# Kernel optimization log

Hardware: AMD Instinct MI355X
Metric: run time of the kernel (lower is better)

Reference implementation:

```python
import jax, jax.numpy as jnp
import numpy as np

NUM_HEADS = 16


def setup_inputs() -> dict:
    key = jax.random.key(0)
    ks = jax.random.split(key, 9)
    B, Nq, Nk = 2, 2048, 2048
    qd, kd, vd = 1024, 1024, 1024
    s = 0.02
    return {
        "query": jax.random.normal(ks[0], (B, Nq, qd), jnp.float32),
        "key": jax.random.normal(ks[1], (B, Nk, kd), jnp.float32),
        "value": jax.random.normal(ks[2], (B, Nk, vd), jnp.float32),
        "Wq": jax.random.normal(ks[3], (qd, qd), jnp.float32) * s,
        "bq": jnp.zeros((qd,), jnp.float32),
        "Wk": jax.random.normal(ks[4], (kd, qd), jnp.float32) * s,
        "bk": jnp.zeros((qd,), jnp.float32),
        "Wv": jax.random.normal(ks[5], (vd, vd), jnp.float32) * s,
        "bv": jnp.zeros((vd,), jnp.float32),
    }


def _split_heads(x, num_heads):
    B, N, D = x.shape
    return x.reshape(B, N, num_heads, D // num_heads).transpose(0, 2, 1, 3)  # [B,H,N,depth]


def reference(query, key, value, Wq, bq, Wk, bk, Wv, bv):
    H = NUM_HEADS
    q = _split_heads(query @ Wq + bq, H)   # [B,H,Nq,dq]
    k = _split_heads(key @ Wk + bk, H)     # [B,H,Nk,dq]
    v = _split_heads(value @ Wv + bv, H)   # [B,H,Nk,dv]
    q_depth = q.shape[-1]
    scores = jnp.einsum('bhqd,bhkd->bhqk', q, k) / jnp.sqrt(jnp.float32(q_depth))
    scores = scores - jnp.max(scores, axis=-1, keepdims=True)
    attn = jax.nn.softmax(scores, axis=-1)  # [B,H,Nq,Nk]
    context = jnp.einsum('bhqk,bhkd->bhqd', attn, v)
    B, _, Nq, dv = context.shape
    context = context.transpose(0, 2, 1, 3).reshape(B, Nq, H * dv)
    return (context, attn)
```

## Files before the change

### kernel.cpp

```cpp
#include <hip/hip_runtime.h>
#include <hip/hip_bf16.h>
#include <stdint.h>

typedef __attribute__((ext_vector_type(4))) float floatx4;
typedef __attribute__((ext_vector_type(8))) short shortx8;

#define NTOK 2048
#define DMODEL 1024
#define NHEAD 16
#define DHEAD 64
#define BATCH 2

static __device__ __forceinline__ unsigned short f2bf(float f) {
    union { float f; unsigned int u; } v; v.f = f;
    return (unsigned short)((v.u + 0x7FFFu + ((v.u >> 16) & 1u)) >> 16);
}

static __device__ __forceinline__ floatx4 mfma16(shortx8 a, shortx8 b, floatx4 c) {
    return __builtin_amdgcn_mfma_f32_16x16x32_bf16(a, b, c, 0, 0, 0);
}

static __device__ __forceinline__ void gl_lds16(const unsigned short* g, unsigned short* l) {
    __builtin_amdgcn_global_load_lds(
        (const __attribute__((address_space(1))) unsigned int*)g,
        (__attribute__((address_space(3))) unsigned int*)l, 16, 0, 0);
}

#define C1 0.18033688f

__global__ void cast_x_kernel(const float* __restrict__ q, const float* __restrict__ k,
                              const float* __restrict__ v,
                              unsigned short* __restrict__ oq, unsigned short* __restrict__ ok,
                              unsigned short* __restrict__ ov) {
    const float* src = blockIdx.y == 0 ? q : (blockIdx.y == 1 ? k : v);
    unsigned short* dst = blockIdx.y == 0 ? oq : (blockIdx.y == 1 ? ok : ov);
    int i = (blockIdx.x * 256 + threadIdx.x) * 8;
    floatx4 a = *(const floatx4*)(src + i);
    floatx4 b = *(const floatx4*)(src + i + 4);
    union { shortx8 s; unsigned short u[8]; } o;
    o.u[0] = f2bf(a[0]); o.u[1] = f2bf(a[1]); o.u[2] = f2bf(a[2]); o.u[3] = f2bf(a[3]);
    o.u[4] = f2bf(b[0]); o.u[5] = f2bf(b[1]); o.u[6] = f2bf(b[2]); o.u[7] = f2bf(b[3]);
    *(shortx8*)(dst + i) = o.s;
}

__global__ void transpose_w_kernel(const float* __restrict__ wq, const float* __restrict__ wk,
                                   const float* __restrict__ wv,
                                   unsigned short* __restrict__ tq, unsigned short* __restrict__ tk,
                                   unsigned short* __restrict__ tv) {
    __shared__ float tile[32][33];
    const float* W = blockIdx.z == 0 ? wq : (blockIdx.z == 1 ? wk : wv);
    unsigned short* T = blockIdx.z == 0 ? tq : (blockIdx.z == 1 ? tk : tv);
    int tx = threadIdx.x, ty = threadIdx.y;
    int bx = blockIdx.x, by = blockIdx.y;
#pragma unroll
    for (int j = 0; j < 4; j++)
        tile[ty + j * 8][tx] = W[(by * 32 + ty + j * 8) * DMODEL + bx * 32 + tx];
    __syncthreads();
#pragma unroll
    for (int j = 0; j < 4; j++)
        T[(bx * 32 + ty + j * 8) * DMODEL + by * 32 + tx] = f2bf(tile[tx][ty + j * 8]);
}

__launch_bounds__(256)
__global__ void proj_gemm_kernel(const unsigned short* __restrict__ xq, const unsigned short* __restrict__ xk,
                                 const unsigned short* __restrict__ xv,
                                 const unsigned short* __restrict__ tq, const unsigned short* __restrict__ tk,
                                 const unsigned short* __restrict__ tv,
                                 const float* __restrict__ bq, const float* __restrict__ bk,
                                 const float* __restrict__ bv,
                                 unsigned short* __restrict__ qh, unsigned short* __restrict__ kh,
                                 unsigned short* __restrict__ vt) {
    int z = blockIdx.z;
    const unsigned short* X = z == 0 ? xq : (z == 1 ? xk : xv);
    const unsigned short* W = z == 0 ? tq : (z == 1 ? tk : tv);
    const float* bias = z == 0 ? bq : (z == 1 ? bk : bv);

    __shared__ unsigned short As[128 * 32];
    __shared__ unsigned short Bs[128 * 32];

    int t = threadIdx.x;
    int lane = t & 63, w = t >> 6;
    int wr = w >> 1, wc = w & 1;
    int r = lane & 15, g = lane >> 4;
    int m0 = blockIdx.y * 128, n0 = blockIdx.x * 128;

    floatx4 acc[4][4];
#pragma unroll
    for (int i = 0; i < 4; i++)
#pragma unroll
        for (int j = 0; j < 4; j++) acc[i][j] = (floatx4){0.f, 0.f, 0.f, 0.f};

    for (int kt = 0; kt < DMODEL; kt += 32) {
#pragma unroll
        for (int i = 0; i < 2; i++) {
            int idx = t + 256 * i;
            int row = idx >> 2, c8 = (idx & 3) * 8;
            gl_lds16(X + (size_t)(m0 + row) * DMODEL + kt + c8, As + idx * 8);
            gl_lds16(W + (size_t)(n0 + row) * DMODEL + kt + c8, Bs + idx * 8);
        }
        __syncthreads();
        shortx8 a[4], b[4];
#pragma unroll
        for (int f = 0; f < 4; f++) {
            a[f] = *(const shortx8*)(As + (wr * 64 + f * 16 + r) * 32 + g * 8);
            b[f] = *(const shortx8*)(Bs + (wc * 64 + f * 16 + r) * 32 + g * 8);
        }
#pragma unroll
        for (int fm = 0; fm < 4; fm++)
#pragma unroll
            for (int fn = 0; fn < 4; fn++)
                acc[fm][fn] = mfma16(a[fm], b[fn], acc[fm][fn]);
        __syncthreads();
    }

    unsigned short* dstQK = (z == 0) ? qh : kh;
#pragma unroll
    for (int fm = 0; fm < 4; fm++) {
#pragma unroll
        for (int fn = 0; fn < 4; fn++) {
            int n = n0 + wc * 64 + fn * 16 + r;
            float bval = bias[n];
            int h = n >> 6, d = n & 63;
#pragma unroll
            for (int reg = 0; reg < 4; reg++) {
                int m = m0 + wr * 64 + fm * 16 + g * 4 + reg;
                int bb = m >> 11, tok = m & 2047;
                unsigned short o = f2bf(acc[fm][fn][reg] + bval);
                if (z < 2)
                    dstQK[(((size_t)(bb * NHEAD + h) * NTOK + tok) * DHEAD) + d] = o;
                else
                    vt[(((size_t)(bb * NHEAD + h) * DHEAD + d) * NTOK) + tok] = o;
            }
        }
    }
}

__launch_bounds__(256, 4)
__global__ void attn_fused_kernel(const unsigned short* __restrict__ Qh,
                                  const unsigned short* __restrict__ Kh,
                                  const unsigned short* __restrict__ Vt,
                                  float* __restrict__ ctx, float* __restrict__ attn) {
    __shared__ __align__(16) unsigned short Kst[2][4096];
    __shared__ __align__(16) unsigned short Aux[2][4096];

    int t = threadIdx.x, lane = t & 63, w = t >> 6, r = lane & 15, g = lane >> 4;

    int bid = blockIdx.y * 64 + blockIdx.x;
    int xcd = bid & 7;
    int j = bid >> 3;
    int bh = xcd * 4 + (j & 3);
    int rest = j >> 2;
    int qb = rest >> 1;
    int role = rest & 1;

    int q0 = qb * 64 + w * 16;
    int qrow = q0 + r;
    int rs = r & 7;

    const unsigned short* Qp = Qh + ((size_t)bh * NTOK + q0) * DHEAD;
    const unsigned short* Kbase = Kh + (size_t)bh * NTOK * DHEAD;
    const unsigned short* Vbase = Vt + (size_t)bh * DHEAD * NTOK;

    shortx8 qf0 = *(const shortx8*)(Qp + r * DHEAD + g * 8);
    shortx8 qf1 = *(const shortx8*)(Qp + r * DHEAD + 32 + g * 8);

    const floatx4 zero = (floatx4){0.f, 0.f, 0.f, 0.f};

    auto STK = [&](int b, int it) {
#pragma unroll
        for (int p = 0; p < 2; ++p) {
            int row = p * 32 + (t >> 3);
            int cb = (t & 7) ^ ((t >> 3) & 7);
            gl_lds16(Kbase + ((size_t)(it * 64 + row)) * DHEAD + cb * 8,
                     Kst[b] + p * 2048 + t * 8);
        }
    };
    auto STV = [&](int b, int it) {
#pragma unroll
        for (int p = 0; p < 2; ++p) {
            int row = p * 32 + (t >> 3);
            int cb = (t & 7) ^ ((t >> 3) & 7);
            gl_lds16(Vbase + (size_t)row * NTOK + it * 64 + cb * 8,
                     Aux[b] + p * 2048 + t * 8);
        }
    };
    auto KF = [&](int b, int tq, int h) -> shortx8 {
        return *(const shortx8*)(Kst[b] + (tq * 16 + r) * 64 + 8 * (((h * 4) + g) ^ rs));
    };
    auto VF = [&](int b, int dt, int h4) -> shortx8 {
        return *(const shortx8*)(Aux[b] + (dt * 16 + r) * 64 + 8 * ((h4 + g) ^ rs));
    };

    if (role == 0) {
        floatx4 pv0 = zero, pv1 = zero, pv2 = zero, pv3 = zero;
        float sm = 0.f;
        const bool hi = (g >= 2);
        const int srcA = (r + ((g & 1) << 5)) << 2;
        const int srcB = srcA + 64;

        STK(0, 0); STV(0, 0);
        __syncthreads();
        for (int it = 0; it < 32; ++it) {
            int cur = it & 1, nxt = cur ^ 1;
            if (it < 31) { STK(nxt, it + 1); STV(nxt, it + 1); }
#pragma unroll
            for (int half = 0; half < 2; ++half) {
                unsigned int p01t0, p23t0, p01t1, p23t1;
                {
                    floatx4 sc = mfma16(KF(cur, half * 2, 0), qf0, zero);
                    sc = mfma16(KF(cur, half * 2, 1), qf1, sc);
                    float e0 = exp2f(C1 * sc[0]), e1 = exp2f(C1 * sc[1]);
                    float e2 = exp2f(C1 * sc[2]), e3 = exp2f(C1 * sc[3]);
                    sm += (e0 + e1) + (e2 + e3);
                    asm("v_cvt_pk_bf16_f32 %0, %1, %2" : "=v"(p01t0) : "v"(e0), "v"(e1));
                    asm("v_cvt_pk_bf16_f32 %0, %1, %2" : "=v"(p23t0) : "v"(e2), "v"(e3));
                }
                {
                    floatx4 sc = mfma16(KF(cur, half * 2 + 1, 0), qf0, zero);
                    sc = mfma16(KF(cur, half * 2 + 1, 1), qf1, sc);
                    float e0 = exp2f(C1 * sc[0]), e1 = exp2f(C1 * sc[1]);
                    float e2 = exp2f(C1 * sc[2]), e3 = exp2f(C1 * sc[3]);
                    sm += (e0 + e1) + (e2 + e3);
                    asm("v_cvt_pk_bf16_f32 %0, %1, %2" : "=v"(p01t1) : "v"(e0), "v"(e1));
                    asm("v_cvt_pk_bf16_f32 %0, %1, %2" : "=v"(p23t1) : "v"(e2), "v"(e3));
                }
                int b0a = __builtin_amdgcn_ds_bpermute(srcA, (int)p01t0);
                int b0b = __builtin_amdgcn_ds_bpermute(srcA, (int)p01t1);
                int b1a = __builtin_amdgcn_ds_bpermute(srcA, (int)p23t0);
                int b1b = __builtin_amdgcn_ds_bpermute(srcA, (int)p23t1);
                int b2a = __builtin_amdgcn_ds_bpermute(srcB, (int)p01t0);
                int b2b = __builtin_amdgcn_ds_bpermute(srcB, (int)p01t1);
                int b3a = __builtin_amdgcn_ds_bpermute(srcB, (int)p23t0);
                int b3b = __builtin_amdgcn_ds_bpermute(srcB, (int)p23t1);
                union { unsigned int u[4]; shortx8 s8; } pbu;
                pbu.u[0] = (unsigned)(hi ? b0b : b0a);
                pbu.u[1] = (unsigned)(hi ? b1b : b1a);
                pbu.u[2] = (unsigned)(hi ? b2b : b2a);
                pbu.u[3] = (unsigned)(hi ? b3b : b3a);
                pv0 = mfma16(VF(cur, 0, half * 4), pbu.s8, pv0);
                pv1 = mfma16(VF(cur, 1, half * 4), pbu.s8, pv1);
                pv2 = mfma16(VF(cur, 2, half * 4), pbu.s8, pv2);
                pv3 = mfma16(VF(cur, 3, half * 4), pbu.s8, pv3);
            }
            __syncthreads();
        }
        float tot = sm;
        tot += __shfl_xor(tot, 16, 64);
        tot += __shfl_xor(tot, 32, 64);
        float inv = 1.0f / tot;
        float* ctx_row =
            ctx + ((size_t)((bh >> 4) * NTOK + qrow)) * DMODEL + (bh & 15) * DHEAD + g * 4;
        *(floatx4*)(ctx_row) = pv0 * inv;
        *(floatx4*)(ctx_row + 16) = pv1 * inv;
        *(floatx4*)(ctx_row + 32) = pv2 * inv;
        *(floatx4*)(ctx_row + 48) = pv3 * inv;
    } else {
        float sm = 0.f;
        STK(0, 0);
        __syncthreads();
        for (int it = 0; it < 32; ++it) {
            int cur = it & 1, nxt = cur ^ 1;
            if (it < 31) STK(nxt, it + 1);
#pragma unroll
            for (int tq = 0; tq < 4; ++tq) {
                floatx4 sc = mfma16(KF(cur, tq, 0), qf0, zero);
                sc = mfma16(KF(cur, tq, 1), qf1, sc);
                sm += (exp2f(C1 * sc[0]) + exp2f(C1 * sc[1])) +
                      (exp2f(C1 * sc[2]) + exp2f(C1 * sc[3]));
            }
            __syncthreads();
        }
        float tot = sm;
        tot += __shfl_xor(tot, 16, 64);
        tot += __shfl_xor(tot, 32, 64);
        float nl2s = -__log2f(tot);

        float(*pw)[64] = (float(*)[64])((char*)Aux + (size_t)w * 4096);
        float* attn_base = attn + ((size_t)bh * NTOK + q0) * NTOK;

        STK(0, 0);
        asm volatile("s_waitcnt vmcnt(0)" ::: "memory");
        __builtin_amdgcn_sched_barrier(0);
        __builtin_amdgcn_s_barrier();
        __builtin_amdgcn_sched_barrier(0);

        for (int it = 0; it < 32; ++it) {
            int cur = it & 1, nxt = cur ^ 1;
            if (it < 31) STK(nxt, it + 1);
            int kk0 = it * 64;
#pragma unroll
            for (int tq = 0; tq < 4; ++tq) {
                floatx4 sc = mfma16(KF(cur, tq, 0), qf0, zero);
                sc = mfma16(KF(cur, tq, 1), qf1, sc);
                float e0 = exp2f(fmaf(C1, sc[0], nl2s));
                float e1 = exp2f(fmaf(C1, sc[1], nl2s));
                float e2 = exp2f(fmaf(C1, sc[2], nl2s));
                float e3 = exp2f(fmaf(C1, sc[3], nl2s));
                int x_ = (tq * 4 + g) ^ r;
                *(floatx4*)&pw[r][4 * x_] = (floatx4){e0, e1, e2, e3};
            }
#pragma unroll
            for (int sID = 0; sID < 4; ++sID) {
                int row = 4 * sID + g;
                floatx4 vvv = *(const floatx4*)&pw[row][4 * (r ^ row)];
                __builtin_nontemporal_store(
                    vvv, (floatx4*)(attn_base + (size_t)row * NTOK + kk0 + 4 * r));
            }
            if (it < 31) {
                asm volatile("s_waitcnt vmcnt(4)" ::: "memory");
                __builtin_amdgcn_sched_barrier(0);
                __builtin_amdgcn_s_barrier();
                __builtin_amdgcn_sched_barrier(0);
            }
        }
    }
}

extern "C" void kernel_launch(void* const* d_in, const int* in_sizes, int n_in,
                              void* d_out, int out_size, void* d_ws, size_t ws_size,
                              hipStream_t stream) {
    const float* query = (const float*)d_in[0];
    const float* key   = (const float*)d_in[1];
    const float* value = (const float*)d_in[2];
    const float* Wq = (const float*)d_in[3];
    const float* bq = (const float*)d_in[4];
    const float* Wk = (const float*)d_in[5];
    const float* bk = (const float*)d_in[6];
    const float* Wv = (const float*)d_in[7];
    const float* bv = (const float*)d_in[8];

    const size_t NX = (size_t)BATCH * NTOK * DMODEL;
    const size_t NW = (size_t)DMODEL * DMODEL;

    unsigned short* ws = (unsigned short*)d_ws;
    unsigned short* Xq = ws;
    unsigned short* Xk = Xq + NX;
    unsigned short* Xv = Xk + NX;
    unsigned short* Tq = Xv + NX;
    unsigned short* Tk = Tq + NW;
    unsigned short* Tv = Tk + NW;
    unsigned short* Qh = Tv + NW;
    unsigned short* Kh = Qh + NX;
    unsigned short* Vt = Kh + NX;

    float* ctx = (float*)d_out;
    float* attn = ctx + NX;

    cast_x_kernel<<<dim3(2048, 3), 256, 0, stream>>>(query, key, value, Xq, Xk, Xv);
    transpose_w_kernel<<<dim3(32, 32, 3), dim3(32, 8), 0, stream>>>(Wq, Wk, Wv, Tq, Tk, Tv);
    proj_gemm_kernel<<<dim3(8, 32, 3), 256, 0, stream>>>(Xq, Xk, Xv, Tq, Tk, Tv,
                                                         bq, bk, bv, Qh, Kh, Vt);
    attn_fused_kernel<<<dim3(64, 32), 256, 0, stream>>>(Qh, Kh, Vt, ctx, attn);
}
```

Baseline: 249.6 us.

## Merge attn-writer blocks to handle two query tiles per block

The attention-probability writer blocks now each cover two 64-row query tiles. The row-sum pass computes both tiles' scores from a single K stream, and two write passes follow. The grid shrinks from 2048 to 1536 blocks: 1024 context blocks and 512 writer blocks. This halves the extra K reads and barriers in the sum pass and balances work between the two roles, at the cost of more register pressure and fewer blocks to spread across CUs.

```diff
diff --git a/kernel.cpp b/kernel.cpp
--- a/kernel.cpp
+++ b/kernel.cpp
@@ -145,24 +145,16 @@
 
     int t = threadIdx.x, lane = t & 63, w = t >> 6, r = lane & 15, g = lane >> 4;
 
-    int bid = blockIdx.y * 64 + blockIdx.x;
+    int bid = blockIdx.x;
     int xcd = bid & 7;
     int j = bid >> 3;
     int bh = xcd * 4 + (j & 3);
-    int rest = j >> 2;
-    int qb = rest >> 1;
-    int role = rest & 1;
-
-    int q0 = qb * 64 + w * 16;
-    int qrow = q0 + r;
+    int unit = j >> 2;
+
     int rs = r & 7;
 
-    const unsigned short* Qp = Qh + ((size_t)bh * NTOK + q0) * DHEAD;
     const unsigned short* Kbase = Kh + (size_t)bh * NTOK * DHEAD;
     const unsigned short* Vbase = Vt + (size_t)bh * DHEAD * NTOK;
-
-    shortx8 qf0 = *(const shortx8*)(Qp + r * DHEAD + g * 8);
-    shortx8 qf1 = *(const shortx8*)(Qp + r * DHEAD + 32 + g * 8);
 
     const floatx4 zero = (floatx4){0.f, 0.f, 0.f, 0.f};
 
@@ -191,7 +183,13 @@
         return *(const shortx8*)(Aux[b] + (dt * 16 + r) * 64 + 8 * ((h4 + g) ^ rs));
     };
 
-    if (role == 0) {
+    if (unit < 32) {
+        int q0 = unit * 64 + w * 16;
+        int qrow = q0 + r;
+        const unsigned short* Qp = Qh + ((size_t)bh * NTOK + q0) * DHEAD;
+        shortx8 qf0 = *(const shortx8*)(Qp + r * DHEAD + g * 8);
+        shortx8 qf1 = *(const shortx8*)(Qp + r * DHEAD + 32 + g * 8);
+
         floatx4 pv0 = zero, pv1 = zero, pv2 = zero, pv3 = zero;
         float sm = 0.f;
         const bool hi = (g >= 2);
@@ -255,7 +253,18 @@
         *(floatx4*)(ctx_row + 32) = pv2 * inv;
         *(floatx4*)(ctx_row + 48) = pv3 * inv;
     } else {
-        float sm = 0.f;
+        int pr = unit - 32;
+        int q0a = (pr * 2) * 64 + w * 16;
+        int q0b = q0a + 64;
+
+        const unsigned short* Qpa = Qh + ((size_t)bh * NTOK + q0a) * DHEAD;
+        const unsigned short* Qpb = Qh + ((size_t)bh * NTOK + q0b) * DHEAD;
+        shortx8 qf0a = *(const shortx8*)(Qpa + r * DHEAD + g * 8);
+        shortx8 qf1a = *(const shortx8*)(Qpa + r * DHEAD + 32 + g * 8);
+        shortx8 qf0b = *(const shortx8*)(Qpb + r * DHEAD + g * 8);
+        shortx8 qf1b = *(const shortx8*)(Qpb + r * DHEAD + 32 + g * 8);
+
+        float sma = 0.f, smb = 0.f;
         STK(0, 0);
         __syncthreads();
         for (int it = 0; it < 32; ++it) {
@@ -263,55 +272,72 @@
             if (it < 31) STK(nxt, it + 1);
 #pragma unroll
             for (int tq = 0; tq < 4; ++tq) {
-                floatx4 sc = mfma16(KF(cur, tq, 0), qf0, zero);
-                sc = mfma16(KF(cur, tq, 1), qf1, sc);
-                sm += (exp2f(C1 * sc[0]) + exp2f(C1 * sc[1])) +
-                      (exp2f(C1 * sc[2]) + exp2f(C1 * sc[3]));
+                floatx4 sa = mfma16(KF(cur, tq, 0), qf0a, zero);
+                sa = mfma16(KF(cur, tq, 1), qf1a, sa);
+                floatx4 sb = mfma16(KF(cur, tq, 0), qf0b, zero);
+                sb = mfma16(KF(cur, tq, 1), qf1b, sb);
+                sma += (exp2f(C1 * sa[0]) + exp2f(C1 * sa[1])) +
+                       (exp2f(C1 * sa[2]) + exp2f(C1 * sa[3]));
+                smb += (exp2f(C1 * sb[0]) + exp2f(C1 * sb[1])) +
+                       (exp2f(C1 * sb[2]) + exp2f(C1 * sb[3]));
             }
             __syncthreads();
         }
-        float tot = sm;
-        tot += __shfl_xor(tot, 16, 64);
-        tot += __shfl_xor(tot, 32, 64);
-        float nl2s = -__log2f(tot);
+        float tota = sma, totb = smb;
+        tota += __shfl_xor(tota, 16, 64);
+        tota += __shfl_xor(tota, 32, 64);
+        totb += __shfl_xor(totb, 16, 64);
+        totb += __shfl_xor(totb, 32, 64);
+        float nl2sa = -__log2f(tota);
+        float nl2sb = -__log2f(totb);
 
         float(*pw)[64] = (float(*)[64])((char*)Aux + (size_t)w * 4096);
-        float* attn_base = attn + ((size_t)bh * NTOK + q0) * NTOK;
-
-        STK(0, 0);
-        asm volatile("s_waitcnt vmcnt(0)" ::: "memory");
-        __builtin_amdgcn_sched_barrier(0);
-        __builtin_amdgcn_s_barrier();
-        __builtin_amdgcn_sched_barrier(0);
-
-        for (int it = 0; it < 32; ++it) {
-            int cur = it & 1, nxt = cur ^ 1;
-            if (it < 31) STK(nxt, it + 1);
-            int kk0 = it * 64;
-#pragma unroll
-            for (int tq = 0; tq < 4; ++tq) {
-                floatx4 sc = mfma16(KF(cur, tq, 0), qf0, zero);
-                sc = mfma16(KF(cur, tq, 1), qf1, sc);
-                float e0 = exp2f(fmaf(C1, sc[0], nl2s));
-                float e1 = exp2f(fmaf(C1, sc[1], nl2s));
-                float e2 = exp2f(fmaf(C1, sc[2], nl2s));
-                float e3 = exp2f(fmaf(C1, sc[3], nl2s));
-                int x_ = (tq * 4 + g) ^ r;
-                *(floatx4*)&pw[r][4 * x_] = (floatx4){e0, e1, e2, e3};
+
+#pragma unroll 1
+        for (int half = 0; half < 2; ++half) {
+            int q0 = half == 0 ? q0a : q0b;
+            float nl2s = half == 0 ? nl2sa : nl2sb;
+            float* attn_base = attn + ((size_t)bh * NTOK + q0) * NTOK;
+
+            STK(0, 0);
+            asm volatile("s_waitcnt vmcnt(0)" ::: "memory");
+            __builtin_amdgcn_sched_barrier(0);
+            __builtin_amdgcn_s_barrier();
+            __builtin_amdgcn_sched_barrier(0);
+
+            for (int it = 0; it < 32; ++it) {
+                int cur = it & 1, nxt = cur ^ 1;
+                if (it < 31) STK(nxt, it + 1);
+                int kk0 = it * 64;
+#pragma unroll
+                for (int tq = 0; tq < 4; ++tq) {
+                    floatx4 sc = mfma16(KF(cur, tq, 0), half == 0 ? qf0a : qf0b, zero);
+                    sc = mfma16(KF(cur, tq, 1), half == 0 ? qf1a : qf1b, sc);
+                    float e0 = exp2f(fmaf(C1, sc[0], nl2s));
+                    float e1 = exp2f(fmaf(C1, sc[1], nl2s));
+                    float e2 = exp2f(fmaf(C1, sc[2], nl2s));
+                    float e3 = exp2f(fmaf(C1, sc[3], nl2s));
+                    int x_ = (tq * 4 + g) ^ r;
+                    *(floatx4*)&pw[r][4 * x_] = (floatx4){e0, e1, e2, e3};
+                }
+#pragma unroll
+                for (int sID = 0; sID < 4; ++sID) {
+                    int row = 4 * sID + g;
+                    floatx4 vvv = *(const floatx4*)&pw[row][4 * (r ^ row)];
+                    __builtin_nontemporal_store(
+                        vvv, (floatx4*)(attn_base + (size_t)row * NTOK + kk0 + 4 * r));
+                }
+                if (it < 31) {
+                    asm volatile("s_waitcnt vmcnt(4)" ::: "memory");
+                    __builtin_amdgcn_sched_barrier(0);
+                    __builtin_amdgcn_s_barrier();
+                    __builtin_amdgcn_sched_barrier(0);
+                }
             }
-#pragma unroll
-            for (int sID = 0; sID < 4; ++sID) {
-                int row = 4 * sID + g;
-                floatx4 vvv = *(const floatx4*)&pw[row][4 * (r ^ row)];
-                __builtin_nontemporal_store(
-                    vvv, (floatx4*)(attn_base + (size_t)row * NTOK + kk0 + 4 * r));
-            }
-            if (it < 31) {
-                asm volatile("s_waitcnt vmcnt(4)" ::: "memory");
-                __builtin_amdgcn_sched_barrier(0);
-                __builtin_amdgcn_s_barrier();
-                __builtin_amdgcn_sched_barrier(0);
-            }
+            asm volatile("s_waitcnt vmcnt(0)" ::: "memory");
+            __builtin_amdgcn_sched_barrier(0);
+            __builtin_amdgcn_s_barrier();
+            __builtin_amdgcn_sched_barrier(0);
         }
     }
 }
@@ -350,5 +376,5 @@
     transpose_w_kernel<<<dim3(32, 32, 3), dim3(32, 8), 0, stream>>>(Wq, Wk, Wv, Tq, Tk, Tv);
     proj_gemm_kernel<<<dim3(8, 32, 3), 256, 0, stream>>>(Xq, Xk, Xv, Tq, Tk, Tv,
                                                          bq, bk, bv, Qh, Kh, Vt);
-    attn_fused_kernel<<<dim3(64, 32), 256, 0, stream>>>(Qh, Kh, Vt, ctx, attn);
-}
+    attn_fused_kernel<<<dim3(1536), 256, 0, stream>>>(Qh, Kh, Vt, ctx, attn);
+}
```

Measured after the change: 301.1 us. 1.21x slower.
